# Kernel tuning notes

Hardware: AMD Instinct MI355X
Metric: run time of the kernel (lower is better)

The kernel has to match this reference:

```python
import jax, jax.numpy as jnp
import numpy as np

B, DIM, IN_DIM, H, W = 4, 256, 128, 128, 128
DD = IN_DIM // 2          # down_dim = 64
HEADS = 8
BN_EPS = 1e-5


def conv2d(x, w, b=None, pad=0, dil=1):
    y = jax.lax.conv_general_dilated(
        x, w, window_strides=(1, 1),
        padding=[(pad, pad), (pad, pad)],
        rhs_dilation=(dil, dil),
        dimension_numbers=('NCHW', 'OIHW', 'NCHW'))
    if b is not None:
        y = y + b[None, :, None, None]
    return y


def bn_relu(x, s, o):
    # eval-mode BatchNorm2d with running_mean=0, running_var=1
    return jax.nn.relu(x * (s / np.sqrt(1.0 + BN_EPS))[None, :, None, None] + o[None, :, None, None])


def setup_inputs() -> dict:
    ks = iter(jax.random.split(jax.random.key(0), 80))

    def w(shape, sc=0.05):
        return sc * jax.random.normal(next(ks), shape, jnp.float32)

    def s(c):
        return 1.0 + 0.1 * jax.random.normal(next(ks), (c,), jnp.float32)

    def o(c):
        return 0.02 * jax.random.normal(next(ks), (c,), jnp.float32)

    d = {}
    d['x'] = jax.random.normal(next(ks), (B, DIM, H, W), jnp.float32)
    d['w_dc'] = w((IN_DIM, DIM, 3, 3)); d['b_dc'] = w((IN_DIM,)); d['s_dc'] = s(IN_DIM); d['o_dc'] = o(IN_DIM)
    d['w1'] = w((DD, IN_DIM, 1, 1)); d['b1'] = w((DD,)); d['s1'] = s(DD); d['o1'] = o(DD)
    d['w2'] = w((DD, DD, 3, 3)); d['b2'] = w((DD,)); d['s2'] = s(DD); d['o2'] = o(DD)
    d['w3'] = w((DD, DD, 3, 3)); d['b3'] = w((DD,)); d['s3'] = s(DD); d['o3'] = o(DD)
    d['w4'] = w((DD, DD, 3, 3)); d['b4'] = w((DD,)); d['s4'] = s(DD); d['o4'] = o(DD)
    d['w5'] = w((DD, IN_DIM, 1, 1)); d['b5'] = w((DD,)); d['s5'] = s(DD); d['o5'] = o(DD)
    d['temperature'] = jnp.ones((HEADS, 1, 1), jnp.float32)
    d['w_po'] = w((DD, 2 * DD, 1, 1))  # project_out, bias=False
    d['w_wa'] = w((DD // 16, DD, 1, 1)); d['b_wa'] = w((DD // 16,)); d['s_wa'] = s(DD // 16); d['o_wa'] = o(DD // 16)
    d['w_wb'] = w((DD, DD // 16, 1, 1)); d['b_wb'] = w((DD,))
    d['w_f'] = w((DD, 5 * DD, 1, 1)); d['b_f'] = w((DD,)); d['s_f'] = s(DD); d['o_f'] = o(DD)
    d['w_oa'] = w((DD // 2, DD, 3, 3)); d['b_oa'] = w((DD // 2,)); d['s_oa'] = s(DD // 2); d['o_oa'] = o(DD // 2)
    d['w_ob'] = w((1, DD // 2, 1, 1)); d['b_ob'] = w((1,))
    return d


def reference(x, w_dc, b_dc, s_dc, o_dc, w1, b1, s1, o1, w2, b2, s2, o2,
              w3, b3, s3, o3, w4, b4, s4, o4, w5, b5, s5, o5,
              temperature, w_po, w_wa, b_wa, s_wa, o_wa, w_wb, b_wb,
              w_f, b_f, s_f, o_f, w_oa, b_oa, s_oa, o_oa, w_ob, b_ob):

    def branch(c):
        b, ch, h, wd = c.shape
        f = jnp.fft.fft2(c)                                   # [b,ch,h,w] complex64 (q=k=v=tepqkv)
        qkv = f.reshape(b, HEADS, ch // HEADS, h * wd)        # v (unnormalized)
        n = jnp.sqrt(jnp.sum(jnp.square(jnp.abs(qkv)), axis=-1, keepdims=True))
        qn = qkv / jnp.maximum(n, 1e-12)                      # F.normalize(dim=-1); q == k
        attn = jnp.einsum('bhcn,bhdn->bhcd', qn, qn) * temperature
        # custom complex normalization: separate real/imag softmax
        attn = jax.lax.complex(jax.nn.softmax(attn.real, axis=-1),
                               jax.nn.softmax(attn.imag, axis=-1))
        of = jnp.abs(jnp.fft.ifft2(jnp.einsum('bhcd,bhdn->bhcn', attn, qkv)))  # ifft2 over (c, hw)
        of = of.reshape(b, ch, h, wd)
        g = jax.nn.sigmoid(conv2d(bn_relu(conv2d(f.real, w_wa, b_wa), s_wa, o_wa), w_wb, b_wb))
        ol = jnp.abs(jnp.fft.ifft2(g * f))                    # ifft2 over (h, w)
        return conv2d(jnp.concatenate([of, ol], axis=1), w_po) + c

    xd = bn_relu(conv2d(x, w_dc, b_dc, pad=1), s_dc, o_dc)
    c1 = bn_relu(conv2d(xd, w1, b1), s1, o1)
    c2 = bn_relu(conv2d(c1, w2, b2, pad=3, dil=3), s2, o2)
    F2 = branch(c2)
    c3 = bn_relu(conv2d(c1 + F2, w3, b3, pad=5, dil=5), s3, o3)
    F3 = branch(c3)
    c4 = bn_relu(conv2d(c1 + F3, w4, b4, pad=7, dil=7), s4, o4)
    F4 = branch(c4)
    # conv5: global avg pool -> 1x1 conv -> bilinear upsample of a 1x1 map == broadcast
    c5 = bn_relu(conv2d(jnp.mean(xd, axis=(2, 3), keepdims=True), w5, b5), s5, o5)
    c5 = jnp.broadcast_to(c5, (c5.shape[0], c5.shape[1], xd.shape[2], xd.shape[3]))
    fused = bn_relu(conv2d(jnp.concatenate([c1, F2, F3, F4, c5], axis=1), w_f, b_f), s_f, o_f)
    return conv2d(bn_relu(conv2d(fused, w_oa, b_oa, pad=1), s_oa, o_oa), w_ob, b_ob)
```

## Files before the change

### kernel.cpp

```cpp
#include <hip/hip_runtime.h>

#define S 16384
#define PI_F 3.14159265358979f

struct Ptrs { const float* p[43]; };

enum : int {
  O_SBDC=0, O_SB1=256, O_SB2=512, O_SB3=768, O_SB4=1024, O_SB5=1280,
  O_SBWA=1536, O_SBF=1792, O_SBOA=2048,
  O_M=2304, O_C5=2816, O_NRM=3072, O_GRAM=3328, O_ATT2=7424, O_BEFF=11520,
  O_WB=16384,
  O_PART=147456,
  O_H=180224,
  O_WP=442368,
  O_A=524288,
  O_FIN=8912896,
  O_CC=25690112,
  O_DRE=29884416, O_DIMG=34078720,
  O_ERE=38273024, O_EIM=42467328,
  O_G=46661632
};

typedef short bfrag __attribute__((ext_vector_type(8)));
typedef float ffrag __attribute__((ext_vector_type(4)));

__device__ __forceinline__ float bf2f(unsigned short u){
  union { unsigned int i; float f; } v; v.i = ((unsigned int)u) << 16; return v.f;
}
__device__ __forceinline__ unsigned short f2bf(float f){
  unsigned int x = __float_as_uint(f);
  unsigned int r = x + 0x7fffu + ((x >> 16) & 1u);
  return (unsigned short)(r >> 16);
}

__global__ void prep_sb_kernel(Ptrs P, float* ws){
  const float r = rsqrtf(1.0f + 1e-5f);
  int bi=0, si=0, oi=0, C=0, dst=0;
  switch (blockIdx.x){
    case 0: bi=2; si=3; oi=4; C=128; dst=O_SBDC; break;
    case 1: bi=6; si=7; oi=8; C=64; dst=O_SB1; break;
    case 2: bi=10; si=11; oi=12; C=64; dst=O_SB2; break;
    case 3: bi=14; si=15; oi=16; C=64; dst=O_SB3; break;
    case 4: bi=18; si=19; oi=20; C=64; dst=O_SB4; break;
    case 5: bi=22; si=23; oi=24; C=64; dst=O_SB5; break;
    case 6: bi=28; si=29; oi=30; C=4;  dst=O_SBWA; break;
    case 7: bi=34; si=35; oi=36; C=64; dst=O_SBF; break;
    default: bi=38; si=39; oi=40; C=32; dst=O_SBOA; break;
  }
  for (int c = threadIdx.x; c < C; c += 256){
    float bb = P.p[bi][c], ss = P.p[si][c], oo = P.p[oi][c];
    float sc = ss * r;
    ws[dst + c] = sc;
    ws[dst + C + c] = bb * sc + oo;
  }
}

__global__ __launch_bounds__(256) void xpad_kernel(const float* __restrict__ x,
    unsigned short* __restrict__ XT){
  int yy = blockIdx.x, b = blockIdx.y;
  long obase = ((long)(b*130) + yy) * (130L*256);
  int tid = threadIdx.x;
  if (yy == 0 || yy == 129){
    uint4 z; z.x=0; z.y=0; z.z=0; z.w=0;
    for (int i = tid; i < 130*256/8; i += 256)
      *(uint4*)(XT + obase + (long)i*8) = z;
    return;
  }
  __shared__ float LT[64][129];
  int y = yy - 1;
  for (int c0 = 0; c0 < 256; c0 += 64){
    for (int idx = tid; idx < 64*128; idx += 256){
      int ci = idx >> 7, xx = idx & 127;
      LT[ci][xx] = x[((long)(b*256 + c0 + ci)*128 + y)*128 + xx];
    }
    __syncthreads();
    for (int idx = tid; idx < 128*16; idx += 256){
      int xp = idx >> 4, c4 = (idx & 15)*4;
      ushort4 v;
      v.x = f2bf(LT[c4][xp]);   v.y = f2bf(LT[c4+1][xp]);
      v.z = f2bf(LT[c4+2][xp]); v.w = f2bf(LT[c4+3][xp]);
      *(ushort4*)(XT + obase + (long)(xp+1)*256 + c0 + c4) = v;
    }
    __syncthreads();
  }
  if (tid < 64){
    ushort4 z; z.x=0; z.y=0; z.z=0; z.w=0;
    *(ushort4*)(XT + obase + tid*4) = z;
    *(ushort4*)(XT + obase + 129L*256 + tid*4) = z;
  }
}

__global__ void wt_kernel(const float* __restrict__ w, unsigned short* __restrict__ WH,
    unsigned short* __restrict__ WL){
  for (int e = blockIdx.x*256 + threadIdx.x; e < 294912; e += gridDim.x*256){
    int c32 = e & 31, co = (e >> 5) & 127, kc = (e >> 12) & 7, sh = e >> 15;
    int ky = sh / 3, kx = sh - ky*3;
    int ci = kc*32 + c32;
    float v = w[((long)(co*256 + ci)*3 + ky)*3 + kx];
    unsigned short h = f2bf(v);
    WH[e] = h;
    WL[e] = f2bf(v - bf2f(h));
  }
}

__global__ void wtg_kernel(Ptrs P, unsigned short* __restrict__ WB){
  const float* w; int cout; long off;
  switch (blockIdx.y){
    case 0: w = P.p[9];  cout = 64; off = 0;      break;
    case 1: w = P.p[13]; cout = 64; off = 73728;  break;
    case 2: w = P.p[17]; cout = 64; off = 147456; break;
    default: w = P.p[37]; cout = 32; off = 221184; break;
  }
  int total = 576*cout;
  unsigned short* WH = WB + off;
  unsigned short* WL = WH + total;
  for (int e = blockIdx.x*256 + threadIdx.x; e < total; e += gridDim.x*256){
    int c32 = e & 31;
    int co = (e >> 5) & (cout - 1);
    int kc = (e / (32*cout)) & 1;
    int sh = e / (64*cout);
    int ky = sh/3, kx = sh - ky*3;
    int ci = kc*32 + c32;
    float v = w[((long)(co*64 + ci)*3 + ky)*3 + kx];
    unsigned short h = f2bf(v);
    WH[e] = h;
    WL[e] = f2bf(v - bf2f(h));
  }
}

__global__ void wtp_kernel(Ptrs P, unsigned short* __restrict__ WP){
  const float* w; int KC, wstr; long off;
  switch (blockIdx.y){
    case 0: w = P.p[5];  KC = 4; wstr = 128; off = 0;     break;
    case 1: w = P.p[26]; KC = 4; wstr = 128; off = 16384; break;
    default: w = P.p[33]; KC = 8; wstr = 320; off = 32768; break;
  }
  int total = KC*64*32;
  unsigned short* WH = WP + off;
  unsigned short* WL = WH + total;
  for (int e = blockIdx.x*256 + threadIdx.x; e < total; e += gridDim.x*256){
    int c32 = e & 31, co = (e >> 5) & 63, kc = e >> 11;
    float v = w[(long)co*wstr + kc*32 + c32];
    unsigned short h = f2bf(v);
    WH[e] = h;
    WL[e] = f2bf(v - bf2f(h));
  }
}

template<int DIL>
__global__ __launch_bounds__(256) void xpad64_kernel(const float* __restrict__ in1,
    const float* __restrict__ in2, long in_bs, unsigned short* __restrict__ XP){
  constexpr int TW = 128 + 2*DIL;
  int yy = blockIdx.x, b = blockIdx.y;
  long obase = (long)(b*TW + yy) * TW * 64;
  int tid = threadIdx.x;
  if (yy < DIL || yy >= 128 + DIL){
    uint4 z; z.x=0; z.y=0; z.z=0; z.w=0;
    for (int i = tid; i < TW*8; i += 256)
      *(uint4*)(XP + obase + (long)i*8) = z;
    return;
  }
  __shared__ float LT[64][129];
  int y = yy - DIL;
  const float* p1 = in1 + (long)b*in_bs + (long)y*128;
  const float* p2 = in2 ? in2 + (long)b*in_bs + (long)y*128 : nullptr;
  for (int idx = tid; idx < 64*128; idx += 256){
    int ci = idx >> 7, xx = idx & 127;
    float v = p1[(long)ci*S + xx];
    if (p2) v += p2[(long)ci*S + xx];
    LT[ci][xx] = v;
  }
  __syncthreads();
  for (int i = tid; i < 2*DIL*16; i += 256){
    int side = i / (DIL*16);
    int r = i - side*(DIL*16);
    int xcol = side ? (128 + DIL + (r >> 4)) : (r >> 4);
    ushort4 z; z.x=0; z.y=0; z.z=0; z.w=0;
    *(ushort4*)(XP + obase + (long)xcol*64 + (r & 15)*4) = z;
  }
  for (int idx = tid; idx < 128*16; idx += 256){
    int xp = idx >> 4, c4 = (idx & 15)*4;
    ushort4 v;
    v.x = f2bf(LT[c4][xp]);   v.y = f2bf(LT[c4+1][xp]);
    v.z = f2bf(LT[c4+2][xp]); v.w = f2bf(LT[c4+3][xp]);
    *(ushort4*)(XP + obase + (long)(xp + DIL)*64 + c4) = v;
  }
}

template<int DIL, int KC, int NBLK>
__global__ __launch_bounds__(256) void conv3x3_mfma_kernel(
    const unsigned short* __restrict__ XP,
    const unsigned short* __restrict__ WH, const unsigned short* __restrict__ WL,
    const float* __restrict__ scbi, float* __restrict__ out){
  constexpr int CIN = KC*32;
  constexpr int TW = 128 + 2*DIL;
  constexpr int NJ = NBLK/32;
  constexpr int LDA = 36;
  constexpr int NSTG = (TW + 63)/64;
  constexpr int NS = 3*KC;
  __shared__ unsigned short As[2][TW*LDA];
  int bid = blockIdx.x;
  int y = (bid & 7)*16 + ((bid >> 3) & 15);
  int b = (bid >> 7) & 3;
  int n2 = bid >> 9;
  int nb = gridDim.x >> 9; if (nb == 0) nb = 1;
  int coutTotal = nb * NBLK;
  int tid = threadIdx.x, wv = tid >> 6, lane = tid & 63;
  int mhalf = wv & 1, nhalf = wv >> 1;
  int px0 = mhalf*64;
  ffrag acc[4][NJ];
  #pragma unroll
  for (int i = 0; i < 4; i++)
    #pragma unroll
    for (int j = 0; j < NJ; j++)
      #pragma unroll
      for (int r = 0; r < 4; r++) acc[i][j][r] = 0.f;

  int kq = (lane >> 4)*8, rown = lane & 15;
  int sx = tid >> 2, sq = tid & 3;
  int cobase = n2*NBLK + nhalf*(NBLK/2);

  {
    long rowbase = ((long)(b*TW + y))*TW*CIN + sq*8;
    #pragma unroll
    for (int t = 0; t < NSTG; t++){
      int x = sx + 64*t;
      int xc = x < TW ? x : TW - 1;
      uint4 v = *(const uint4*)(XP + rowbase + (long)xc*CIN);
      if (x < TW) *(uint4*)&As[0][x*LDA + sq*8] = v;
    }
  }
  __syncthreads();

  for (int s = 0; s < NS; s++){
    int cur = s & 1;
    int ky = s / KC, kc = s - ky*KC;
    int s2 = (s + 1 < NS) ? s + 1 : s;
    int ky2 = s2 / KC, kc2 = s2 - ky2*KC;
    uint4 pre[NSTG];
    {
      long rowbase = ((long)(b*TW + y + ky2*DIL))*TW*CIN + kc2*32 + sq*8;
      #pragma unroll
      for (int t = 0; t < NSTG; t++){
        int x = sx + 64*t;
        int xc = x < TW ? x : TW - 1;
        pre[t] = *(const uint4*)(XP + rowbase + (long)xc*CIN);
      }
    }
    #pragma unroll
    for (int kx = 0; kx < 3; kx++){
      int step = (ky*3 + kx)*KC + kc;
      bfrag bhf[NJ], blf[NJ];
      #pragma unroll
      for (int j = 0; j < NJ; j++){
        long wb = ((long)step*coutTotal + cobase + j*16 + rown)*32 + kq;
        bhf[j] = *(const bfrag*)(WH + wb);
        blf[j] = *(const bfrag*)(WL + wb);
      }
      bfrag af[4];
      #pragma unroll
      for (int i = 0; i < 4; i++){
        int x = px0 + i*16 + rown + kx*DIL;
        af[i] = *(const bfrag*)&As[cur][x*LDA + kq];
      }
      #pragma unroll
      for (int i = 0; i < 4; i++)
        #pragma unroll
        for (int j = 0; j < NJ; j++){
          acc[i][j] = __builtin_amdgcn_mfma_f32_16x16x32_bf16(af[i], blf[j], acc[i][j], 0, 0, 0);
          acc[i][j] = __builtin_amdgcn_mfma_f32_16x16x32_bf16(af[i], bhf[j], acc[i][j], 0, 0, 0);
        }
    }
    #pragma unroll
    for (int t = 0; t < NSTG; t++){
      int x = sx + 64*t;
      if (x < TW) *(uint4*)&As[cur ^ 1][x*LDA + sq*8] = pre[t];
    }
    __syncthreads();
  }
  #pragma unroll
  for (int i = 0; i < 4; i++){
    int pixel = px0 + i*16 + (lane >> 4)*4;
    #pragma unroll
    for (int j = 0; j < NJ; j++){
      int co = cobase + j*16 + (lane & 15);
      float sc = scbi[co], bb = scbi[coutTotal + co];
      float* op = out + ((long)(b*coutTotal + co))*S + y*128 + pixel;
      #pragma unroll
      for (int r = 0; r < 4; r++)
        op[r] = fmaxf(acc[i][j][r]*sc + bb, 0.f);
    }
  }
}

template<int MODE, int KC, int BF16IN>
__global__ __launch_bounds__(256) void conv1x1_mfma_kernel(
    const void* __restrict__ inv, long in_bs,
    const unsigned short* __restrict__ WH, const unsigned short* __restrict__ WL,
    const float* __restrict__ scbi, const float* __restrict__ beff,
    const float* __restrict__ res, long res_bs,
    float* __restrict__ out, long out_bs){
  constexpr int LDA = 36;
  __shared__ unsigned short Als[128*LDA];
  __shared__ unsigned short BHs[64*LDA];
  __shared__ unsigned short BLs[64*LDA];
  int bid = blockIdx.x;
  int y = (bid & 7)*16 + ((bid >> 3) & 15);
  int b = bid >> 7;
  int tid = threadIdx.x, wv = tid >> 6, lane = tid & 63;
  int mt0 = (wv & 1)*4, nt0 = (wv >> 1)*2;
  ffrag acc[4][2];
  #pragma unroll
  for (int i = 0; i < 4; i++)
    #pragma unroll
    for (int j = 0; j < 2; j++)
      #pragma unroll
      for (int r = 0; r < 4; r++) acc[i][j][r] = 0.f;
  int pq = tid & 31, cg = tid >> 5;
  int kq = (lane >> 4)*8, rown = lane & 15;
  int wrB = (tid >> 2)*LDA + (tid & 3)*8;
  const float* ibf = (const float*)inv + (long)b*in_bs + y*128;
  const unsigned short* ibs = (const unsigned short*)inv + (long)b*in_bs + y*128;
  unsigned short a[16];
  uint4 BHr, BLr;
  #pragma unroll
  for (int cc = 0; cc < 4; cc++)
    #pragma unroll
    for (int i = 0; i < 4; i++){
      if (BF16IN) a[cc*4 + i] = ibs[(long)(cg*4 + cc)*S + pq + 32*i];
      else        a[cc*4 + i] = f2bf(ibf[(long)(cg*4 + cc)*S + pq + 32*i]);
    }
  BHr = *(const uint4*)(WH + tid*8);
  BLr = *(const uint4*)(WL + tid*8);
  for (int kc = 0; kc < KC; kc++){
    __syncthreads();
    #pragma unroll
    for (int i = 0; i < 4; i++){
      ushort4 v;
      v.x = a[0 + i];  v.y = a[4 + i];
      v.z = a[8 + i];  v.w = a[12 + i];
      *(ushort4*)&Als[(pq + 32*i)*LDA + cg*4] = v;
    }
    *(uint4*)&BHs[wrB] = BHr;
    *(uint4*)&BLs[wrB] = BLr;
    __syncthreads();
    if (kc + 1 < KC){
      #pragma unroll
      for (int cc = 0; cc < 4; cc++)
        #pragma unroll
        for (int i = 0; i < 4; i++){
          long off = (long)((kc + 1)*32 + cg*4 + cc)*S + pq + 32*i;
          if (BF16IN) a[cc*4 + i] = ibs[off];
          else        a[cc*4 + i] = f2bf(ibf[off]);
        }
      long gw = (long)(kc + 1)*2048;
      BHr = *(const uint4*)(WH + gw + tid*8);
      BLr = *(const uint4*)(WL + gw + tid*8);
    }
    bfrag af[4], bhf[2], blf[2];
    #pragma unroll
    for (int i = 0; i < 4; i++)
      af[i] = *(const bfrag*)&Als[((mt0 + i)*16 + rown)*LDA + kq];
    #pragma unroll
    for (int j = 0; j < 2; j++){
      bhf[j] = *(const bfrag*)&BHs[((nt0 + j)*16 + rown)*LDA + kq];
      blf[j] = *(const bfrag*)&BLs[((nt0 + j)*16 + rown)*LDA + kq];
    }
    #pragma unroll
    for (int i = 0; i < 4; i++)
      #pragma unroll
      for (int j = 0; j < 2; j++){
        acc[i][j] = __builtin_amdgcn_mfma_f32_16x16x32_bf16(af[i], blf[j], acc[i][j], 0, 0, 0);
        acc[i][j] = __builtin_amdgcn_mfma_f32_16x16x32_bf16(af[i], bhf[j], acc[i][j], 0, 0, 0);
      }
  }
  #pragma unroll
  for (int i = 0; i < 4; i++){
    int pixel = (mt0 + i)*16 + (lane >> 4)*4;
    #pragma unroll
    for (int j = 0; j < 2; j++){
      int co = (nt0 + j)*16 + (lane & 15);
      float* op = out + (long)b*out_bs + (long)co*S + y*128 + pixel;
      #pragma unroll
      for (int r = 0; r < 4; r++){
        float v = acc[i][j][r];
        if (MODE == 0){
          v = fmaxf(v*scbi[co] + scbi[64 + co], 0.f);
        } else if (MODE == 1){
          v += res[(long)b*res_bs + (long)co*S + y*128 + pixel + r];
        } else {
          v = fmaxf(v*scbi[co] + beff[b*64 + co], 0.f);
        }
        op[r] = v;
      }
    }
  }
}

__device__ __forceinline__ void fft128_mk_tw(float (&tws)[8], float (&twc)[8],
                                             float sign, int lane){
  float a0 = sign * (2.0f*PI_F/128.0f) * (float)lane;
  __sincosf(a0, &tws[0], &twc[0]);
  int i = 1;
  #pragma unroll
  for (int h = 32; h >= 1; h >>= 1, i++){
    int j = lane & (h - 1);
    float a = sign * (2.0f*PI_F/128.0f) * (float)(j * (64/h));
    __sincosf(a, &tws[i], &twc[i]);
  }
}

__device__ __forceinline__ void fft128(float& z0r, float& z0i, float& z1r, float& z1i,
    const float (&tws)[8], const float (&twc)[8], int lane){
  {
    float ar = z0r, ai = z0i, br = z1r, bi = z1i;
    z0r = ar + br; z0i = ai + bi;
    float dr = ar - br, di = ai - bi;
    float s = tws[0], c = twc[0];
    z1r = dr*c - di*s; z1i = dr*s + di*c;
  }
  int idx = 1;
  #pragma unroll
  for (int h = 32; h >= 1; h >>= 1, idx++){
    float s = tws[idx], c = twc[idx];
    bool up = (lane & h) != 0;
    float pr, pi, nr, ni;
    pr = __shfl_xor(z0r, h, 64); pi = __shfl_xor(z0i, h, 64);
    if (!up){ nr = z0r + pr; ni = z0i + pi; }
    else { float dr = pr - z0r, di = pi - z0i; nr = dr*c - di*s; ni = dr*s + di*c; }
    z0r = nr; z0i = ni;
    pr = __shfl_xor(z1r, h, 64); pi = __shfl_xor(z1i, h, 64);
    if (!up){ nr = z1r + pr; ni = z1i + pi; }
    else { float dr = pr - z1r, di = pi - z1i; nr = dr*c - di*s; ni = dr*s + di*c; }
    z1r = nr; z1i = ni;
  }
}


__global__ __launch_bounds__(1024) void fft2_fwd_kernel(const float* __restrict__ in,
    unsigned short* __restrict__ outRe, unsigned short* __restrict__ outIm){
  __shared__ float lre[128][129];
  __shared__ float lim[128][129];
  int plane = blockIdx.x;
  int tid = threadIdx.x, wv = tid >> 6, lane = tid & 63;
  long pbase = (long)plane * S;
  for (int i = tid; i < S/4; i += 1024){
    int px = i*4; int r = px >> 7, c = px & 127;
    float4 v = *(const float4*)(in + pbase + px);
    lre[r][c] = v.x; lre[r][c+1] = v.y; lre[r][c+2] = v.z; lre[r][c+3] = v.w;
  }
  float tws[8], twc[8];
  fft128_mk_tw(tws, twc, -1.0f, lane);
  __syncthreads();
  #pragma unroll
  for (int rr = 0; rr < 8; rr++){
    int r = wv*8 + rr;
    float z0r = lre[r][lane], z0i = 0.f;
    float z1r = lre[r][lane + 64], z1i = 0.f;
    fft128(z0r, z0i, z1r, z1i, tws, twc, lane);
    int k = __brev(lane) >> 25;
    lre[r][k] = z0r;     lim[r][k] = z0i;
    lre[r][k+1] = z1r;   lim[r][k+1] = z1i;
  }
  __syncthreads();
  #pragma unroll
  for (int cc = 0; cc < 8; cc++){
    int c = wv*8 + cc;
    float z0r = lre[lane][c], z0i = lim[lane][c];
    float z1r = lre[lane + 64][c], z1i = lim[lane + 64][c];
    fft128(z0r, z0i, z1r, z1i, tws, twc, lane);
    int k = __brev(lane) >> 25;
    lre[k][c] = z0r;     lim[k][c] = z0i;
    lre[k+1][c] = z1r;   lim[k+1][c] = z1i;
  }
  __syncthreads();
  for (int i = tid; i < S/2; i += 1024){
    int px = i*2; int r = px >> 7, c = px & 127;
    ushort2 vr, vi;
    vr.x = f2bf(lre[r][c]); vr.y = f2bf(lre[r][c+1]);
    vi.x = f2bf(lim[r][c]); vi.y = f2bf(lim[r][c+1]);
    *(ushort2*)(outRe + pbase + px) = vr;
    *(ushort2*)(outIm + pbase + px) = vi;
  }
}

__global__ __launch_bounds__(1024) void ifft2_gate_abs_ol_kernel(
    const unsigned short* __restrict__ Dre, const unsigned short* __restrict__ Dim,
    const float* __restrict__ H, const float* __restrict__ wb, const float* __restrict__ bwb,
    unsigned short* __restrict__ AB){
  __shared__ float lre[128][129];
  __shared__ float lim[128][129];
  int plane = blockIdx.x;
  int b = plane >> 6, ch = plane & 63;
  int tid = threadIdx.x, wv = tid >> 6, lane = tid & 63;
  long pbase = (long)plane * S;
  float w0 = wb[ch*4], w1 = wb[ch*4+1], w2 = wb[ch*4+2], w3 = wb[ch*4+3];
  float bw = bwb[ch];
  const float* Hb = H + (long)b*4*S;
  for (int i = tid; i < S; i += 1024){
    int r = i >> 7, c = i & 127;
    float hv = bw + w0*Hb[i] + w1*Hb[S + i] + w2*Hb[2*S + i] + w3*Hb[3*S + i];
    float g = 1.0f / (1.0f + __expf(-hv));
    lre[r][c] = bf2f(Dre[pbase + i]) * g;
    lim[r][c] = bf2f(Dim[pbase + i]) * g;
  }
  float tws[8], twc[8];
  fft128_mk_tw(tws, twc, 1.0f, lane);
  __syncthreads();
  #pragma unroll
  for (int cc = 0; cc < 8; cc++){
    int c = wv*8 + cc;
    float z0r = lre[lane][c], z0i = lim[lane][c];
    float z1r = lre[lane + 64][c], z1i = lim[lane + 64][c];
    fft128(z0r, z0i, z1r, z1i, tws, twc, lane);
    int k = __brev(lane) >> 25;
    lre[k][c] = z0r;     lim[k][c] = z0i;
    lre[k+1][c] = z1r;   lim[k+1][c] = z1i;
  }
  __syncthreads();
  unsigned short* out = AB + ((long)(b*128 + 64 + ch)) * S;
  #pragma unroll
  for (int rr = 0; rr < 8; rr++){
    int r = wv*8 + rr;
    float z0r = lre[r][lane], z0i = lim[r][lane];
    float z1r = lre[r][lane + 64], z1i = lim[r][lane + 64];
    fft128(z0r, z0i, z1r, z1i, tws, twc, lane);
    int k = __brev(lane) >> 25;
    ushort2 v;
    v.x = f2bf(sqrtf(z0r*z0r + z0i*z0i) * (1.0f/16384.0f));
    v.y = f2bf(sqrtf(z1r*z1r + z1i*z1i) * (1.0f/16384.0f));
    *(ushort2*)(out + (long)r*128 + k) = v;
  }
}

__global__ __launch_bounds__(1024) void ifft2_attn_abs_ofT_kernel(
    const unsigned short* __restrict__ Dre, const unsigned short* __restrict__ Dim,
    const float* __restrict__ ATT2, unsigned short* __restrict__ AB){
  __shared__ float lre[128][129];
  __shared__ float lim[128][129];
  int plane = blockIdx.x;
  int b = plane >> 6, ch = plane & 63;
  int bh = plane >> 3;
  int cp = plane & 7;
  int tid = threadIdx.x, wv = tid >> 6, lane = tid & 63;
  long hbase = (long)bh * 8 * S;
  float wr[8], wi[8];
  #pragma unroll
  for (int d = 0; d < 8; d++){
    wr[d] = ATT2[bh*128 + (cp*8 + d)*2];
    wi[d] = ATT2[bh*128 + (cp*8 + d)*2 + 1];
  }
  for (int i = tid; i < S/2; i += 1024){
    int px = i*2;
    float sr0=0.f, si0=0.f, sr1=0.f, si1=0.f;
    #pragma unroll
    for (int d = 0; d < 8; d++){
      ushort2 ur = *(const ushort2*)(Dre + hbase + (long)d*S + px);
      ushort2 ui = *(const ushort2*)(Dim + hbase + (long)d*S + px);
      float xr0 = bf2f(ur.x), xi0 = bf2f(ui.x);
      float xr1 = bf2f(ur.y), xi1 = bf2f(ui.y);
      sr0 += wr[d]*xr0 - wi[d]*xi0;  si0 += wr[d]*xi0 + wi[d]*xr0;
      sr1 += wr[d]*xr1 - wi[d]*xi1;  si1 += wr[d]*xi1 + wi[d]*xr1;
    }
    int r = px >> 7, c = px & 127;
    lre[r][c] = sr0;   lim[r][c] = si0;
    lre[r][c+1] = sr1; lim[r][c+1] = si1;
  }
  float tws[8], twc[8];
  fft128_mk_tw(tws, twc, 1.0f, lane);
  __syncthreads();
  #pragma unroll
  for (int cc = 0; cc < 8; cc++){
    int c = wv*8 + cc;
    float z0r = lre[lane][c], z0i = lim[lane][c];
    float z1r = lre[lane + 64][c], z1i = lim[lane + 64][c];
    fft128(z0r, z0i, z1r, z1i, tws, twc, lane);
    int k = __brev(lane) >> 25;
    float s, co;
    float a0 = (2.0f*PI_F/16384.0f) * (float)(c * k);
    __sincosf(a0, &s, &co);
    float t = z0r*co - z0i*s; z0i = z0r*s + z0i*co; z0r = t;
    float a1 = (2.0f*PI_F/16384.0f) * (float)(c * (k + 1));
    __sincosf(a1, &s, &co);
    t = z1r*co - z1i*s; z1i = z1r*s + z1i*co; z1r = t;
    lre[k][c] = z0r;     lim[k][c] = z0i;
    lre[k+1][c] = z1r;   lim[k+1][c] = z1i;
  }
  __syncthreads();
  float absv[8][2];
  #pragma unroll
  for (int rr = 0; rr < 8; rr++){
    int r = wv*8 + rr;
    float z0r = lre[r][lane], z0i = lim[r][lane];
    float z1r = lre[r][lane + 64], z1i = lim[r][lane + 64];
    fft128(z0r, z0i, z1r, z1i, tws, twc, lane);
    absv[rr][0] = sqrtf(z0r*z0r + z0i*z0i) * (1.0f/16384.0f);
    absv[rr][1] = sqrtf(z1r*z1r + z1i*z1i) * (1.0f/16384.0f);
  }
  __syncthreads();
  int k2 = __brev(lane) >> 25;
  #pragma unroll
  for (int rr = 0; rr < 8; rr++){
    int r = wv*8 + rr;
    lre[k2][r] = absv[rr][0];
    lre[k2+1][r] = absv[rr][1];
  }
  __syncthreads();
  unsigned short* out = AB + ((long)(b*128 + ch)) * S;
  for (int i = tid; i < S/2; i += 1024){
    int px = i*2; int r = px >> 7, c = px & 127;
    ushort2 v;
    v.x = f2bf(lre[r][c]); v.y = f2bf(lre[r][c+1]);
    *(ushort2*)(out + px) = v;
  }
}

__global__ __launch_bounds__(256) void gram_part_kernel(
    const unsigned short* __restrict__ Dre, const unsigned short* __restrict__ Dim,
    float* __restrict__ PART){
  int bh = blockIdx.x, slab = blockIdx.y;
  long base = (long)bh * 8 * S;
  int n0 = slab * 2048;
  float accr[36], acci[36], nsq[8];
  #pragma unroll
  for (int i = 0; i < 36; i++){ accr[i] = 0.f; acci[i] = 0.f; }
  #pragma unroll
  for (int i = 0; i < 8; i++) nsq[i] = 0.f;
  for (int it = 0; it < 8; it++){
    int n = n0 + it*256 + threadIdx.x;
    float xr[8], xi[8];
    #pragma unroll
    for (int c = 0; c < 8; c++){
      xr[c] = bf2f(Dre[base + (long)c*S + n]);
      xi[c] = bf2f(Dim[base + (long)c*S + n]);
      nsq[c] += xr[c]*xr[c] + xi[c]*xi[c];
    }
    int t = 0;
    #pragma unroll
    for (int c = 0; c < 8; c++)
      #pragma unroll
      for (int d = c; d < 8; d++){
        accr[t] += xr[c]*xr[d] - xi[c]*xi[d];
        acci[t] += xr[c]*xi[d] + xi[c]*xr[d];
        t++;
      }
  }
  __shared__ float red[4][80];
  int wv = threadIdx.x >> 6, lane = threadIdx.x & 63;
  #pragma unroll
  for (int i = 0; i < 80; i++){
    float v = (i < 36) ? accr[i] : (i < 72) ? acci[i - 36] : nsq[i - 72];
    #pragma unroll
    for (int o = 32; o; o >>= 1) v += __shfl_xor(v, o, 64);
    if (lane == 0) red[wv][i] = v;
  }
  __syncthreads();
  if (threadIdx.x < 80){
    int i = threadIdx.x;
    PART[(long)(bh*8 + slab)*80 + i] = red[0][i] + red[1][i] + red[2][i] + red[3][i];
  }
}

__global__ void attn2f_kernel(const float* __restrict__ PART,
    const float* __restrict__ temp, float* __restrict__ ATT2){
  __shared__ float ssum[80];
  __shared__ float sar[64], sai[64];
  int bh = blockIdx.x;
  int t = threadIdx.x;
  if (t < 80){
    float s = 0.f;
    for (int i = 0; i < 8; i++) s += PART[(long)(bh*8 + i)*80 + t];
    ssum[t] = s;
  }
  __syncthreads();
  if (t >= 64) return;
  int lane = t;
  int c = lane >> 3, d = lane & 7;
  int lo = min(c, d), hi = max(c, d);
  int t2 = lo*8 - lo*(lo - 1)/2 + (hi - lo);
  float nnc = fmaxf(sqrtf(ssum[72 + c]), 1e-12f);
  float nnd = fmaxf(sqrtf(ssum[72 + d]), 1e-12f);
  float inv = temp[bh & 7] / (nnc * nnd);
  float ar = ssum[t2] * inv, ai = ssum[36 + t2] * inv;
  float m = ar;
  m = fmaxf(m, __shfl_xor(m, 1, 64)); m = fmaxf(m, __shfl_xor(m, 2, 64)); m = fmaxf(m, __shfl_xor(m, 4, 64));
  float e = __expf(ar - m);
  float su = e;
  su += __shfl_xor(su, 1, 64); su += __shfl_xor(su, 2, 64); su += __shfl_xor(su, 4, 64);
  ar = e / su;
  m = ai;
  m = fmaxf(m, __shfl_xor(m, 1, 64)); m = fmaxf(m, __shfl_xor(m, 2, 64)); m = fmaxf(m, __shfl_xor(m, 4, 64));
  e = __expf(ai - m);
  su = e;
  su += __shfl_xor(su, 1, 64); su += __shfl_xor(su, 2, 64); su += __shfl_xor(su, 4, 64);
  ai = e / su;
  sar[lane] = ar; sai[lane] = ai;
  __syncthreads();
  const float ct[8] = {1.f, 0.70710678f, 0.f, -0.70710678f, -1.f, -0.70710678f, 0.f, 0.70710678f};
  const float st[8] = {0.f, 0.70710678f, 1.f, 0.70710678f, 0.f, -0.70710678f, -1.f, -0.70710678f};
  int cp = c;
  float sr = 0.f, si = 0.f;
  #pragma unroll
  for (int cc = 0; cc < 8; cc++){
    int k = (cc * cp) & 7;
    float a = sar[cc*8 + d], b2 = sai[cc*8 + d];
    sr += ct[k]*a - st[k]*b2;
    si += ct[k]*b2 + st[k]*a;
  }
  float2 v; v.x = sr * 0.125f; v.y = si * 0.125f;
  ((float2*)ATT2)[bh*64 + lane] = v;
}

__global__ __launch_bounds__(256) void gateh_kernel(const unsigned short* __restrict__ Dre,
    const float* __restrict__ wa, const float* __restrict__ sbwa, float* __restrict__ H){
  int b = blockIdx.y;
  int px = blockIdx.x*256 + threadIdx.x;
  long base = (long)b * 64 * S + px;
  float h0 = 0.f, h1 = 0.f, h2 = 0.f, h3 = 0.f;
  for (int ci = 0; ci < 64; ci++){
    float x = bf2f(Dre[base + (long)ci*S]);
    h0 += wa[ci]*x; h1 += wa[64 + ci]*x; h2 += wa[128 + ci]*x; h3 += wa[192 + ci]*x;
  }
  long ob = (long)b * 4 * S + px;
  H[ob]       = fmaxf(h0*sbwa[0] + sbwa[4], 0.f);
  H[ob + S]   = fmaxf(h1*sbwa[1] + sbwa[5], 0.f);
  H[ob + 2*S] = fmaxf(h2*sbwa[2] + sbwa[6], 0.f);
  H[ob + 3*S] = fmaxf(h3*sbwa[3] + sbwa[7], 0.f);
}

__global__ __launch_bounds__(256) void mean_kernel(const float* __restrict__ A, float* __restrict__ M){
  int p = blockIdx.x;
  long base = (long)p * S;
  float s = 0.f;
  for (int n = threadIdx.x; n < S; n += 256) s += A[base + n];
  #pragma unroll
  for (int o = 32; o; o >>= 1) s += __shfl_xor(s, o, 64);
  __shared__ float sm[4];
  if ((threadIdx.x & 63) == 0) sm[threadIdx.x >> 6] = s;
  __syncthreads();
  if (threadIdx.x == 0) M[p] = (sm[0] + sm[1] + sm[2] + sm[3]) * (1.0f/16384.0f);
}

__global__ void c5_kernel(const float* __restrict__ W5, const float* __restrict__ sb5,
    const float* __restrict__ M, float* __restrict__ C5){
  int t = threadIdx.x;
  if (t >= 256) return;
  int b = t >> 6, co = t & 63;
  float s = 0.f;
  for (int ci = 0; ci < 128; ci++) s += W5[co*128 + ci] * M[b*128 + ci];
  C5[t] = fmaxf(s * sb5[co] + sb5[64 + co], 0.f);
}

__global__ void beff_kernel(const float* __restrict__ WF, const float* __restrict__ sbf,
    const float* __restrict__ C5, float* __restrict__ BEFF){
  int t = threadIdx.x;
  if (t >= 256) return;
  int b = t >> 6, co = t & 63;
  float s = 0.f;
  for (int j = 0; j < 64; j++) s += WF[co*320 + 256 + j] * C5[b*64 + j];
  BEFF[t] = s * sbf[co] + sbf[64 + co];
}

__global__ __launch_bounds__(256) void ob_kernel(const float* __restrict__ Tin,
    const float* __restrict__ wob, const float* __restrict__ bob, float* __restrict__ out){
  int b = blockIdx.y;
  int px = blockIdx.x*1024 + (threadIdx.x & 63)*4 + (threadIdx.x >> 6)*256;
  float b0 = bob[0];
  float4 a; a.x = b0; a.y = b0; a.z = b0; a.w = b0;
  for (int ci = 0; ci < 32; ci++){
    float4 v = *(const float4*)(Tin + ((long)b*32 + ci)*S + px);
    float w = wob[ci];
    a.x += w*v.x; a.y += w*v.y; a.z += w*v.z; a.w += w*v.w;
  }
  *(float4*)(out + (long)b*S + px) = a;
}

extern "C" void kernel_launch(void* const* d_in, const int* in_sizes, int n_in,
                              void* d_out, int out_size, void* d_ws, size_t ws_size,
                              hipStream_t stream){
  float* ws = (float*)d_ws;
  Ptrs P;
  for (int i = 0; i < 43 && i < n_in; i++) P.p[i] = (const float*)d_in[i];
  float* out = (float*)d_out;

  float* A   = ws + O_A;
  float* FIN = ws + O_FIN;
  float* CC  = ws + O_CC;
  float* G   = ws + O_G;
  float* H   = ws + O_H;

  unsigned short* DRE16 = (unsigned short*)(ws + O_DRE);
  unsigned short* DIM16 = (unsigned short*)(ws + O_DIMG);
  unsigned short* AB    = (unsigned short*)(ws + O_A);

  unsigned short* XT  = (unsigned short*)(ws + O_DRE);
  unsigned short* WHd = (unsigned short*)(ws + O_CC);
  unsigned short* WLd = (unsigned short*)(ws + O_CC + 147456);
  unsigned short* WB  = (unsigned short*)(ws + O_WB);
  unsigned short* WP  = (unsigned short*)(ws + O_WP);
  unsigned short* XP  = (unsigned short*)(ws + O_ERE);

  prep_sb_kernel<<<dim3(9), dim3(256), 0, stream>>>(P, ws);
  xpad_kernel<<<dim3(130, 4), dim3(256), 0, stream>>>(P.p[0], XT);
  wt_kernel<<<dim3(128), dim3(256), 0, stream>>>(P.p[1], WHd, WLd);
  wtg_kernel<<<dim3(16, 4), dim3(256), 0, stream>>>(P, WB);
  wtp_kernel<<<dim3(8, 3), dim3(256), 0, stream>>>(P, WP);

  conv3x3_mfma_kernel<1,8,64><<<dim3(1024), dim3(256), 0, stream>>>(
      XT, WHd, WLd, ws + O_SBDC, A);

  mean_kernel<<<dim3(512), dim3(256), 0, stream>>>(A, ws + O_M);
  c5_kernel<<<dim3(1), dim3(256), 0, stream>>>(P.p[21], ws + O_SB5, ws + O_M, ws + O_C5);
  beff_kernel<<<dim3(1), dim3(256), 0, stream>>>(P.p[33], ws + O_SBF, ws + O_C5, ws + O_BEFF);

  conv1x1_mfma_kernel<0,4,0><<<dim3(512), dim3(256), 0, stream>>>(
      A, 128*S, WP, WP + 8192, ws + O_SB1, nullptr, nullptr, 0, FIN, 256*S);

  for (int k = 0; k < 3; k++){
    const float* sb = ws + (k == 0 ? O_SB2 : k == 1 ? O_SB3 : O_SB4);
    const float* in2 = (k == 0) ? nullptr : FIN + (long)(64*k)*S;
    unsigned short* wh = WB + (k == 0 ? 0 : k == 1 ? 73728 : 147456);
    if (k == 0){
      xpad64_kernel<3><<<dim3(134, 4), dim3(256), 0, stream>>>(FIN, in2, 256*S, XP);
      conv3x3_mfma_kernel<3,2,64><<<dim3(512), dim3(256), 0, stream>>>(
          XP, wh, wh + 36864, sb, CC);
    } else if (k == 1){
      xpad64_kernel<5><<<dim3(138, 4), dim3(256), 0, stream>>>(FIN, in2, 256*S, XP);
      conv3x3_mfma_kernel<5,2,64><<<dim3(512), dim3(256), 0, stream>>>(
          XP, wh, wh + 36864, sb, CC);
    } else {
      xpad64_kernel<7><<<dim3(142, 4), dim3(256), 0, stream>>>(FIN, in2, 256*S, XP);
      conv3x3_mfma_kernel<7,2,64><<<dim3(512), dim3(256), 0, stream>>>(
          XP, wh, wh + 36864, sb, CC);
    }

    fft2_fwd_kernel<<<dim3(256), dim3(1024), 0, stream>>>(CC, DRE16, DIM16);
    gram_part_kernel<<<dim3(32, 8), dim3(256), 0, stream>>>(DRE16, DIM16, ws + O_PART);
    attn2f_kernel<<<dim3(32), dim3(128), 0, stream>>>(ws + O_PART, P.p[25], ws + O_ATT2);
    gateh_kernel<<<dim3(64, 4), dim3(256), 0, stream>>>(DRE16, P.p[27], ws + O_SBWA, H);
    ifft2_gate_abs_ol_kernel<<<dim3(256), dim3(1024), 0, stream>>>(
        DRE16, DIM16, H, P.p[31], P.p[32], AB);
    ifft2_attn_abs_ofT_kernel<<<dim3(256), dim3(1024), 0, stream>>>(
        DRE16, DIM16, ws + O_ATT2, AB);
    conv1x1_mfma_kernel<1,4,1><<<dim3(512), dim3(256), 0, stream>>>(
        AB, 128*S, WP + 16384, WP + 24576, nullptr, nullptr, CC, 64*S,
        FIN + (long)(64*(k + 1))*S, 256*S);
  }

  conv1x1_mfma_kernel<2,8,0><<<dim3(512), dim3(256), 0, stream>>>(
      FIN, 256*S, WP + 32768, WP + 49152, ws + O_SBF, ws + O_BEFF, nullptr, 0, CC, 64*S);
  xpad64_kernel<1><<<dim3(130, 4), dim3(256), 0, stream>>>(CC, nullptr, 64*S, XP);
  conv3x3_mfma_kernel<1,2,32><<<dim3(512), dim3(256), 0, stream>>>(
      XP, WB + 221184, WB + 221184 + 18432, ws + O_SBOA, G);
  ob_kernel<<<dim3(16, 4), dim3(256), 0, stream>>>(G, P.p[41], P.p[42], out);
}
```

Baseline: 924.3 us.

## Vectorize FFT/gram loads, fuse c5 and beff kernels, widen first conv tile

The gate and attention inverse-FFT prologues and the gram partial kernel now load two or four bf16/float elements per access instead of one, which cuts the number of memory instructions. The c5 and beff kernels are merged into one launch that passes the intermediate through shared memory. The first 3x3 conv switches its template tile parameter from 64 to 128 and halves its grid. The wider vector loads raise register pressure, and the larger conv tile cuts the number of blocks, which may leave fewer workgroups per CU.

Result: no change. 924.6 us (+0.0%).

```diff
diff --git a/kernel.cpp b/kernel.cpp
--- a/kernel.cpp
+++ b/kernel.cpp
@@ -497,12 +497,21 @@
   float w0 = wb[ch*4], w1 = wb[ch*4+1], w2 = wb[ch*4+2], w3 = wb[ch*4+3];
   float bw = bwb[ch];
   const float* Hb = H + (long)b*4*S;
-  for (int i = tid; i < S; i += 1024){
-    int r = i >> 7, c = i & 127;
-    float hv = bw + w0*Hb[i] + w1*Hb[S + i] + w2*Hb[2*S + i] + w3*Hb[3*S + i];
-    float g = 1.0f / (1.0f + __expf(-hv));
-    lre[r][c] = bf2f(Dre[pbase + i]) * g;
-    lim[r][c] = bf2f(Dim[pbase + i]) * g;
+  for (int i = tid; i < S/2; i += 1024){
+    int px = i*2;
+    float2 h0 = *(const float2*)(Hb + px);
+    float2 h1 = *(const float2*)(Hb + S + px);
+    float2 h2 = *(const float2*)(Hb + 2*S + px);
+    float2 h3 = *(const float2*)(Hb + 3*S + px);
+    ushort2 ur = *(const ushort2*)(Dre + pbase + px);
+    ushort2 ui = *(const ushort2*)(Dim + pbase + px);
+    float hva = bw + w0*h0.x + w1*h1.x + w2*h2.x + w3*h3.x;
+    float hvb = bw + w0*h0.y + w1*h1.y + w2*h2.y + w3*h3.y;
+    float ga = 1.0f / (1.0f + __expf(-hva));
+    float gb = 1.0f / (1.0f + __expf(-hvb));
+    int r = px >> 7, c = px & 127;
+    lre[r][c]   = bf2f(ur.x) * ga;  lim[r][c]   = bf2f(ui.x) * ga;
+    lre[r][c+1] = bf2f(ur.y) * gb;  lim[r][c+1] = bf2f(ui.y) * gb;
   }
   float tws[8], twc[8];
   fft128_mk_tw(tws, twc, 1.0f, lane);
@@ -550,21 +559,27 @@
     wr[d] = ATT2[bh*128 + (cp*8 + d)*2];
     wi[d] = ATT2[bh*128 + (cp*8 + d)*2 + 1];
   }
-  for (int i = tid; i < S/2; i += 1024){
-    int px = i*2;
-    float sr0=0.f, si0=0.f, sr1=0.f, si1=0.f;
+  for (int i = tid; i < S/4; i += 1024){
+    int px = i*4;
+    float sr0=0.f, si0=0.f, sr1=0.f, si1=0.f, sr2=0.f, si2=0.f, sr3=0.f, si3=0.f;
     #pragma unroll
     for (int d = 0; d < 8; d++){
-      ushort2 ur = *(const ushort2*)(Dre + hbase + (long)d*S + px);
-      ushort2 ui = *(const ushort2*)(Dim + hbase + (long)d*S + px);
+      ushort4 ur = *(const ushort4*)(Dre + hbase + (long)d*S + px);
+      ushort4 ui = *(const ushort4*)(Dim + hbase + (long)d*S + px);
       float xr0 = bf2f(ur.x), xi0 = bf2f(ui.x);
       float xr1 = bf2f(ur.y), xi1 = bf2f(ui.y);
+      float xr2 = bf2f(ur.z), xi2 = bf2f(ui.z);
+      float xr3 = bf2f(ur.w), xi3 = bf2f(ui.w);
       sr0 += wr[d]*xr0 - wi[d]*xi0;  si0 += wr[d]*xi0 + wi[d]*xr0;
       sr1 += wr[d]*xr1 - wi[d]*xi1;  si1 += wr[d]*xi1 + wi[d]*xr1;
+      sr2 += wr[d]*xr2 - wi[d]*xi2;  si2 += wr[d]*xi2 + wi[d]*xr2;
+      sr3 += wr[d]*xr3 - wi[d]*xi3;  si3 += wr[d]*xi3 + wi[d]*xr3;
     }
     int r = px >> 7, c = px & 127;
-    lre[r][c] = sr0;   lim[r][c] = si0;
-    lre[r][c+1] = sr1; lim[r][c+1] = si1;
+    lre[r][c]   = sr0;  lim[r][c]   = si0;
+    lre[r][c+1] = sr1;  lim[r][c+1] = si1;
+    lre[r][c+2] = sr2;  lim[r][c+2] = si2;
+    lre[r][c+3] = sr3;  lim[r][c+3] = si3;
   }
   float tws[8], twc[8];
   fft128_mk_tw(tws, twc, 1.0f, lane);
@@ -626,22 +641,27 @@
   for (int i = 0; i < 36; i++){ accr[i] = 0.f; acci[i] = 0.f; }
   #pragma unroll
   for (int i = 0; i < 8; i++) nsq[i] = 0.f;
-  for (int it = 0; it < 8; it++){
-    int n = n0 + it*256 + threadIdx.x;
-    float xr[8], xi[8];
+  for (int it = 0; it < 4; it++){
+    int n = n0 + (it*256 + threadIdx.x)*2;
+    float xr[8][2], xi[8][2];
     #pragma unroll
     for (int c = 0; c < 8; c++){
-      xr[c] = bf2f(Dre[base + (long)c*S + n]);
-      xi[c] = bf2f(Dim[base + (long)c*S + n]);
-      nsq[c] += xr[c]*xr[c] + xi[c]*xi[c];
+      ushort2 ur = *(const ushort2*)(Dre + base + (long)c*S + n);
+      ushort2 ui = *(const ushort2*)(Dim + base + (long)c*S + n);
+      xr[c][0] = bf2f(ur.x); xr[c][1] = bf2f(ur.y);
+      xi[c][0] = bf2f(ui.x); xi[c][1] = bf2f(ui.y);
+      nsq[c] += xr[c][0]*xr[c][0] + xi[c][0]*xi[c][0]
+              + xr[c][1]*xr[c][1] + xi[c][1]*xi[c][1];
     }
     int t = 0;
     #pragma unroll
     for (int c = 0; c < 8; c++)
       #pragma unroll
       for (int d = c; d < 8; d++){
-        accr[t] += xr[c]*xr[d] - xi[c]*xi[d];
-        acci[t] += xr[c]*xi[d] + xi[c]*xr[d];
+        accr[t] += xr[c][0]*xr[d][0] - xi[c][0]*xi[d][0]
+                 + xr[c][1]*xr[d][1] - xi[c][1]*xi[d][1];
+        acci[t] += xr[c][0]*xi[d][0] + xi[c][0]*xr[d][0]
+                 + xr[c][1]*xi[d][1] + xi[c][1]*xr[d][1];
         t++;
       }
   }
@@ -741,24 +761,20 @@
   if (threadIdx.x == 0) M[p] = (sm[0] + sm[1] + sm[2] + sm[3]) * (1.0f/16384.0f);
 }
 
-__global__ void c5_kernel(const float* __restrict__ W5, const float* __restrict__ sb5,
-    const float* __restrict__ M, float* __restrict__ C5){
+__global__ void c5beff_kernel(const float* __restrict__ W5, const float* __restrict__ sb5,
+    const float* __restrict__ WF, const float* __restrict__ sbf,
+    const float* __restrict__ M, float* __restrict__ BEFF){
+  __shared__ float c5s[256];
   int t = threadIdx.x;
   if (t >= 256) return;
   int b = t >> 6, co = t & 63;
   float s = 0.f;
   for (int ci = 0; ci < 128; ci++) s += W5[co*128 + ci] * M[b*128 + ci];
-  C5[t] = fmaxf(s * sb5[co] + sb5[64 + co], 0.f);
-}
-
-__global__ void beff_kernel(const float* __restrict__ WF, const float* __restrict__ sbf,
-    const float* __restrict__ C5, float* __restrict__ BEFF){
-  int t = threadIdx.x;
-  if (t >= 256) return;
-  int b = t >> 6, co = t & 63;
-  float s = 0.f;
-  for (int j = 0; j < 64; j++) s += WF[co*320 + 256 + j] * C5[b*64 + j];
-  BEFF[t] = s * sbf[co] + sbf[64 + co];
+  c5s[t] = fmaxf(s * sb5[co] + sb5[64 + co], 0.f);
+  __syncthreads();
+  float s2 = 0.f;
+  for (int j = 0; j < 64; j++) s2 += WF[co*320 + 256 + j] * c5s[b*64 + j];
+  BEFF[t] = s2 * sbf[co] + sbf[64 + co];
 }
 
 __global__ __launch_bounds__(256) void ob_kernel(const float* __restrict__ Tin,
@@ -806,12 +822,12 @@
   wtg_kernel<<<dim3(16, 4), dim3(256), 0, stream>>>(P, WB);
   wtp_kernel<<<dim3(8, 3), dim3(256), 0, stream>>>(P, WP);
 
-  conv3x3_mfma_kernel<1,8,64><<<dim3(1024), dim3(256), 0, stream>>>(
+  conv3x3_mfma_kernel<1,8,128><<<dim3(512), dim3(256), 0, stream>>>(
       XT, WHd, WLd, ws + O_SBDC, A);
 
   mean_kernel<<<dim3(512), dim3(256), 0, stream>>>(A, ws + O_M);
-  c5_kernel<<<dim3(1), dim3(256), 0, stream>>>(P.p[21], ws + O_SB5, ws + O_M, ws + O_C5);
-  beff_kernel<<<dim3(1), dim3(256), 0, stream>>>(P.p[33], ws + O_SBF, ws + O_C5, ws + O_BEFF);
+  c5beff_kernel<<<dim3(1), dim3(256), 0, stream>>>(
+      P.p[21], ws + O_SB5, P.p[33], ws + O_SBF, ws + O_M, ws + O_BEFF);
 
   conv1x1_mfma_kernel<0,4,0><<<dim3(512), dim3(256), 0, stream>>>(
       A, 128*S, WP, WP + 8192, ws + O_SB1, nullptr, nullptr, 0, FIN, 256*S);
```
